# Optimization experiments

Measured on AMD Instinct MI355X. Metric: run time of the kernel, lower is better.

## Reference

```python
import jax, jax.numpy as jnp
import numpy as np

N = 100000          # total nodes
G = 128             # number of graphs
D_IN, D_H, D_OUT = 512, 1024, 512
E = 1600000         # edges (unused by the math, matches forward signature)


def setup_inputs() -> dict:
    key = jax.random.key(0)
    ks = jax.random.split(key, 9)
    x = jax.random.normal(ks[0], (N, D_IN), dtype=jnp.float32)
    edge_index = jax.random.randint(ks[1], (2, E), 0, N, dtype=jnp.int64)
    # sorted batch ids; guarantee every graph id appears at least once
    batch = jnp.sort(jnp.concatenate([
        jnp.arange(G, dtype=jnp.int64),
        jax.random.randint(ks[2], (N - G,), 0, G, dtype=jnp.int64),
    ]))
    s = 0.02
    W0 = jax.random.normal(ks[3], (D_IN, D_H), dtype=jnp.float32) * s
    b0 = jnp.zeros((D_H,), dtype=jnp.float32)
    W1 = jax.random.normal(ks[4], (D_H, D_H), dtype=jnp.float32) * s
    b1 = jnp.zeros((D_H,), dtype=jnp.float32)
    W2 = jax.random.normal(ks[5], (D_H, D_OUT), dtype=jnp.float32) * s
    b2 = jnp.zeros((D_OUT,), dtype=jnp.float32)
    return {"x": x, "edge_index": edge_index, "batch": batch,
            "W0": W0, "b0": b0, "W1": W1, "b1": b1, "W2": W2, "b2": b2}


def reference(x, edge_index, batch, W0, b0, W1, b1, W2, b2):
    # Linear + ReLU stack (dropout p=0 -> identity in eval). edge_index is unused,
    # matching the original module (its 'GCN' layer is a plain nn.Linear).
    h = jax.nn.relu(x @ W0 + b0)
    h = jax.nn.relu(h @ W1 + b1)
    h = jax.nn.relu(h @ W2 + b2)        # [N, D_OUT]
    # global mean pool per graph: fused segment-sum replaces the per-graph mask loop
    sums = jax.ops.segment_sum(h, batch, num_segments=G)                 # [G, D_OUT]
    counts = jax.ops.segment_sum(jnp.ones((h.shape[0],), h.dtype), batch,
                                 num_segments=G)                          # [G]
    return sums / counts[:, None]
```

## Files before the change

### kernel.cpp

```cpp
#include <hip/hip_runtime.h>
#include <cstdint>
#include <cstddef>

typedef __bf16 bf16x8 __attribute__((ext_vector_type(8)));
typedef float f32x4 __attribute__((ext_vector_type(4)));

__device__ __forceinline__ unsigned short f2bf(float f) {
  unsigned u = __float_as_uint(f);
  u += 0x7fffu + ((u >> 16) & 1u);
  return (unsigned short)(u >> 16);
}
__device__ __forceinline__ float bf2f(unsigned short s) {
  return __uint_as_float(((unsigned)s) << 16);
}

__device__ __forceinline__ void gld_lds16(const void* g, void* l) {
  __builtin_amdgcn_global_load_lds(
      (const __attribute__((address_space(1))) void*)g,
      (__attribute__((address_space(3))) void*)l, 16, 0, 0);
}

#define BARM() do { __builtin_amdgcn_s_barrier(); asm volatile("" ::: "memory"); } while (0)
#define VMCNT(n) asm volatile("s_waitcnt vmcnt(" #n ")" ::: "memory")
#define LGKM0()  do { asm volatile("s_waitcnt lgkmcnt(0)" ::: "memory"); \
                      __builtin_amdgcn_sched_barrier(0); } while (0)

__global__ void pack_w(const float* __restrict__ w, unsigned short* __restrict__ wp,
                       int K, int N) {
  __shared__ float tile[32][33];
  int nt32 = N >> 5;
  int bx = blockIdx.x % nt32;
  int by = blockIdx.x / nt32;
  int tx = threadIdx.x & 31, ty = threadIdx.x >> 5;
#pragma unroll
  for (int r = 0; r < 32; r += 8)
    tile[ty + r][tx] = w[(size_t)(by * 32 + ty + r) * N + bx * 32 + tx];
  __syncthreads();
  int KQ = K >> 5;
  int flat = threadIdx.x * 4;
  int c = flat >> 9;
  int l = (flat >> 3) & 63;
  int e0 = flat & 7;
  int nl = c * 16 + (l & 15);
  int kl = (l >> 4) * 8 + e0;
  unsigned short* o = wp + ((size_t)((bx * 2 + c) * KQ + by) * 64 + l) * 8 + e0;
#pragma unroll
  for (int e = 0; e < 4; ++e) o[e] = f2bf(tile[kl + e][nl]);
}

__global__ void cvt_x(const float* __restrict__ x, unsigned short* __restrict__ xb,
                      int rows, int nvalid, int D) {
  size_t total = (size_t)rows * D / 8;
  for (size_t i = (size_t)blockIdx.x * blockDim.x + threadIdx.x; i < total;
       i += (size_t)gridDim.x * blockDim.x) {
    size_t e = i * 8;
    int row = (int)(e / (size_t)D);
    uint4 ov;
    if (row < nvalid) {
      const float4* s = (const float4*)(x + e);
      float4 v0 = s[0], v1 = s[1];
      ov.x = (unsigned)f2bf(v0.x) | ((unsigned)f2bf(v0.y) << 16);
      ov.y = (unsigned)f2bf(v0.z) | ((unsigned)f2bf(v0.w) << 16);
      ov.z = (unsigned)f2bf(v1.x) | ((unsigned)f2bf(v1.y) << 16);
      ov.w = (unsigned)f2bf(v1.z) | ((unsigned)f2bf(v1.w) << 16);
    } else {
      ov.x = ov.y = ov.z = ov.w = 0u;
    }
    *(uint4*)(xb + e) = ov;
  }
}

__device__ __forceinline__ bf16x8 read_frag(const unsigned short* region, int row, int kel) {
  int ke = kel ^ (((row >> 1) & 3) << 3);
  return *(const bf16x8*)(region + row * 32 + ke);
}

__device__ __forceinline__ void stage_a(const unsigned short* gpanel, int K, int kofs,
                                        unsigned short* region, int tid) {
#pragma unroll
  for (int r = 0; r < 4; ++r) {
    int row = r * 64 + (tid >> 2);
    int ke = ((tid & 3) * 8) ^ (((row >> 1) & 3) << 3);
    gld_lds16(gpanel + (size_t)row * K + kofs + ke, region + r * 2048 + tid * 8);
  }
}

__device__ __forceinline__ void load_b4(const unsigned short* wpb, int KQ, int kq, int l,
                                        bf16x8* b) {
#pragma unroll
  for (int nn = 0; nn < 4; ++nn)
    b[nn] = *(const bf16x8*)(wpb + ((size_t)(nn * KQ + kq) * 64 + l) * 8);
}

__global__ __launch_bounds__(256, 2) void gemm_blds(
    const unsigned short* __restrict__ A,
    const unsigned short* __restrict__ Wp,
    const float* __restrict__ bias,
    unsigned short* __restrict__ C,
    int N, int K) {
  __shared__ alignas(16) unsigned short lds[2][8192];
  const int tid = threadIdx.x;
  const int w = tid >> 6, l = tid & 63;
  const int wm = w >> 1, wn = w & 1;
  const int lc = l & 15, lk8 = (l >> 4) * 8;

  const int nbn = N >> 7;
  const int nwg = gridDim.x;
  const int q = nwg >> 3, rr = nwg & 7;
  const int xcd = blockIdx.x & 7, ib = blockIdx.x >> 3;
  const int bswz = (xcd < rr ? xcd * (q + 1) : rr * (q + 1) + (xcd - rr) * q) + ib;
  const int bm = bswz / nbn, bn = bswz - bm * nbn;

  const unsigned short* Ap = A + (size_t)bm * 256 * K;
  const int KQ = K >> 5;
  const unsigned short* wpb = Wp + ((size_t)(bn * 8 + wn * 4) * KQ * 64) * 8;
  const int T = KQ;

  f32x4 acc[8][4] = {};
  bf16x8 a[8], bc[4], bn_[4];

  stage_a(Ap, K, 0, &lds[0][0], tid);
  load_b4(wpb, KQ, 0, l, bc);
  VMCNT(0);
  BARM();

#define TILE_BODY(TT, SRD, SWR, BCUR, BNXT)                                      \
  do {                                                                           \
    _Pragma("unroll") for (int mm = 0; mm < 8; ++mm)                             \
        a[mm] = read_frag(SRD, wm * 128 + mm * 16 + lc, lk8);                    \
    if ((TT) + 1 < T) {                                                          \
      stage_a(Ap, K, ((TT) + 1) * 32, SWR, tid);                                 \
      load_b4(wpb, KQ, (TT) + 1, l, BNXT);                                       \
    }                                                                            \
    BARM();                                                                      \
    LGKM0();                                                                     \
    __builtin_amdgcn_s_setprio(1);                                               \
    _Pragma("unroll") for (int mm = 0; mm < 8; ++mm)                             \
        _Pragma("unroll") for (int nn = 0; nn < 4; ++nn)                         \
            acc[mm][nn] = __builtin_amdgcn_mfma_f32_16x16x32_bf16(               \
                a[mm], BCUR[nn], acc[mm][nn], 0, 0, 0);                          \
    __builtin_amdgcn_s_setprio(0);                                               \
    VMCNT(0);                                                                    \
    BARM();                                                                      \
  } while (0)

  for (int t = 0; t < T; t += 2) {
    TILE_BODY(t, &lds[0][0], &lds[1][0], bc, bn_);
    if (t + 1 < T)
      TILE_BODY(t + 1, &lds[1][0], &lds[0][0], bn_, bc);
  }
#undef TILE_BODY

  unsigned short* eps = &lds[0][0];
  float bv[4];
#pragma unroll
  for (int nn = 0; nn < 4; ++nn) bv[nn] = bias[bn * 128 + wn * 64 + nn * 16 + lc];

#pragma unroll
  for (int r = 0; r < 2; ++r) {
    if (wm == r) {
#pragma unroll
      for (int mm = 0; mm < 8; ++mm) {
#pragma unroll
        for (int nn = 0; nn < 4; ++nn) {
          int lcol = wn * 64 + nn * 16 + lc;
#pragma unroll
          for (int j = 0; j < 4; ++j) {
            int lrow = mm * 16 + (l >> 4) * 4 + j;
            int g = lcol >> 3, e = lcol & 7;
            float v = fmaxf(acc[mm][nn][j] + bv[nn], 0.0f);
            eps[lrow * 128 + ((g ^ (lrow & 15)) << 3) + e] = f2bf(v);
          }
        }
      }
    }
    BARM();
#pragma unroll
    for (int it = 0; it < 8; ++it) {
      int flat = it * 256 + tid;
      int lrow = flat >> 4, cb = flat & 15;
      uint4 v = *(const uint4*)&eps[lrow * 128 + (((cb ^ (lrow & 15))) << 3)];
      *(uint4*)&C[(size_t)(bm * 256 + r * 128 + lrow) * N + bn * 128 + cb * 8] = v;
    }
    BARM();
  }
}

__global__ void pool_partial(const unsigned short* __restrict__ h2, const int* __restrict__ batch,
                             float* __restrict__ part, int n, int D, int S) {
  int g = blockIdx.x / S, sub = blockIdx.x - g * S;
  int lo, hi;
  { int a = 0, b = n; while (a < b) { int m = (a + b) >> 1; if (batch[m] < g) a = m + 1; else b = m; } lo = a; }
  { int a = lo, b = n; while (a < b) { int m = (a + b) >> 1; if (batch[m] < g + 1) a = m + 1; else b = m; } hi = a; }
  int t = threadIdx.x;
  float sx = 0.f, sy = 0.f;
  for (int r = lo + sub; r < hi; r += S) {
    unsigned v = *(const unsigned*)(h2 + (size_t)r * D + t * 2);
    sx += bf2f((unsigned short)(v & 0xffffu));
    sy += bf2f((unsigned short)(v >> 16));
  }
  float* o = part + (size_t)blockIdx.x * D + t * 2;
  o[0] = sx;
  o[1] = sy;
}

__global__ void pool_reduce(const float* __restrict__ part, const int* __restrict__ batch,
                            float* __restrict__ out, int n, int D, int S, int G) {
  int idx = blockIdx.x * blockDim.x + threadIdx.x;
  if (idx >= G * D) return;
  int g = idx / D, d = idx - g * D;
  int lo, hi;
  { int a = 0, b = n; while (a < b) { int m = (a + b) >> 1; if (batch[m] < g) a = m + 1; else b = m; } lo = a; }
  { int a = lo, b = n; while (a < b) { int m = (a + b) >> 1; if (batch[m] < g + 1) a = m + 1; else b = m; } hi = a; }
  float sum = 0.f;
  for (int k = 0; k < S; ++k) sum += part[(size_t)(g * S + k) * D + d];
  out[idx] = sum / (float)(hi - lo);
}

static inline size_t align256(size_t x) { return (x + 255) & ~(size_t)255; }

extern "C" void kernel_launch(void* const* d_in, const int* in_sizes, int n_in,
                              void* d_out, int out_size, void* d_ws, size_t ws_size,
                              hipStream_t stream) {
  const float* x = (const float*)d_in[0];
  const int* batch = (const int*)d_in[2];
  const float* W0 = (const float*)d_in[3];
  const float* b0 = (const float*)d_in[4];
  const float* W1 = (const float*)d_in[5];
  const float* b1 = (const float*)d_in[6];
  const float* W2 = (const float*)d_in[7];
  const float* b2 = (const float*)d_in[8];
  float* out = (float*)d_out;

  const int Nn = in_sizes[2];
  const int DIN = 512, DH = 1024, DOUT = 512;
  const int G = out_size / DOUT;
  const int S = 8;
  const int Mpad = ((Nn + 255) / 256) * 256;

  uint8_t* p = (uint8_t*)d_ws;
  unsigned short* W0p = (unsigned short*)p; p += align256((size_t)DH * DIN * 2);
  unsigned short* W1p = (unsigned short*)p; p += align256((size_t)DH * DH * 2);
  unsigned short* W2p = (unsigned short*)p; p += align256((size_t)DOUT * DH * 2);
  unsigned short* h2  = (unsigned short*)p; p += align256((size_t)Mpad * DOUT * 2);
  float* part         = (float*)p;          p += align256((size_t)G * S * DOUT * 4);
  size_t used = (size_t)(p - (uint8_t*)d_ws);
  size_t avail = ws_size > used ? ws_size - used : 0;
  size_t per_row = (size_t)(DIN + DH + DH) * 2;
  long long chl = (long long)(avail / per_row);
  chl = (chl / 256) * 256;
  int CH = (int)(chl < 256 ? 256 : chl);
  if (CH > Mpad) CH = Mpad;
  unsigned short* xb = (unsigned short*)p; p += align256((size_t)CH * DIN * 2);
  unsigned short* h0 = (unsigned short*)p; p += align256((size_t)CH * DH * 2);
  unsigned short* h1 = (unsigned short*)p; p += align256((size_t)CH * DH * 2);

  pack_w<<<dim3((DH / 32) * (DIN / 32)), 256, 0, stream>>>(W0, W0p, DIN, DH);
  pack_w<<<dim3((DH / 32) * (DH / 32)), 256, 0, stream>>>(W1, W1p, DH, DH);
  pack_w<<<dim3((DOUT / 32) * (DH / 32)), 256, 0, stream>>>(W2, W2p, DH, DOUT);

  for (int off = 0; off < Mpad; off += CH) {
    int rows = Mpad - off; if (rows > CH) rows = CH;
    int nvalid = Nn - off;
    size_t cvt_threads = (size_t)rows * DIN / 8;
    int cvt_blocks = (int)((cvt_threads + 255) / 256);
    if (cvt_blocks > 2048) cvt_blocks = 2048;
    cvt_x<<<dim3(cvt_blocks), 256, 0, stream>>>(x + (size_t)off * DIN, xb, rows, nvalid, DIN);

    gemm_blds<<<dim3((rows / 256) * (DH / 128)), 256, 0, stream>>>(xb, W0p, b0, h0, DH, DIN);
    gemm_blds<<<dim3((rows / 256) * (DH / 128)), 256, 0, stream>>>(h0, W1p, b1, h1, DH, DH);
    gemm_blds<<<dim3((rows / 256) * (DOUT / 128)), 256, 0, stream>>>(
        h1, W2p, b2, h2 + (size_t)off * DOUT, DOUT, DH);
  }

  pool_partial<<<dim3(G * S), 256, 0, stream>>>(h2, batch, part, Nn, DOUT, S);
  pool_reduce<<<dim3((G * DOUT + 255) / 256), 256, 0, stream>>>(part, batch, out, Nn, DOUT, S, G);
}
```

Before: 756.4 us.

## Widen GEMM K-tile to 64 and split B-fragment prefetch within each tile

The bf16 MFMA GEMM now stages a 256x64 A panel per iteration instead of 256x32. The LDS swizzle is adjusted to a row&7 XOR pattern, and the LDS buffers double to 64KB per block. Each iteration runs two 32-wide MFMA passes. The B-fragment register loads are interleaved between them, and fine-grained vmcnt waits replace the old full drain. This cuts barriers and full pipeline stalls per unit of K. The cost is higher LDS use per block, which could limit occupancy, and more delicate wait-count ordering.

```diff
diff --git a/kernel.cpp b/kernel.cpp
--- a/kernel.cpp
+++ b/kernel.cpp
@@ -70,18 +70,18 @@
   }
 }
 
-__device__ __forceinline__ bf16x8 read_frag(const unsigned short* region, int row, int kel) {
-  int ke = kel ^ (((row >> 1) & 3) << 3);
-  return *(const bf16x8*)(region + row * 32 + ke);
-}
-
-__device__ __forceinline__ void stage_a(const unsigned short* gpanel, int K, int kofs,
-                                        unsigned short* region, int tid) {
-#pragma unroll
-  for (int r = 0; r < 4; ++r) {
-    int row = r * 64 + (tid >> 2);
-    int ke = ((tid & 3) * 8) ^ (((row >> 1) & 3) << 3);
-    gld_lds16(gpanel + (size_t)row * K + kofs + ke, region + r * 2048 + tid * 8);
+__device__ __forceinline__ bf16x8 read_frag64(const unsigned short* region, int row, int kel) {
+  int ke = kel ^ ((row & 7) << 3);
+  return *(const bf16x8*)(region + row * 64 + ke);
+}
+
+__device__ __forceinline__ void stage_a64(const unsigned short* gpanel, int K, int kofs,
+                                          unsigned short* region, int tid) {
+#pragma unroll
+  for (int p = 0; p < 8; ++p) {
+    int row = p * 32 + (tid >> 3);
+    int ke = ((tid & 7) * 8) ^ ((row & 7) << 3);
+    gld_lds16(gpanel + (size_t)row * K + kofs + ke, region + p * 2048 + tid * 8);
   }
 }
 
@@ -92,13 +92,23 @@
     b[nn] = *(const bf16x8*)(wpb + ((size_t)(nn * KQ + kq) * 64 + l) * 8);
 }
 
-__global__ __launch_bounds__(256, 2) void gemm_blds(
+#define MFMA32(BV)                                                              \
+  do {                                                                          \
+    __builtin_amdgcn_s_setprio(1);                                              \
+    _Pragma("unroll") for (int mm = 0; mm < 8; ++mm)                            \
+        _Pragma("unroll") for (int nn = 0; nn < 4; ++nn)                        \
+            acc[mm][nn] = __builtin_amdgcn_mfma_f32_16x16x32_bf16(              \
+                a[mm], BV[nn], acc[mm][nn], 0, 0, 0);                           \
+    __builtin_amdgcn_s_setprio(0);                                              \
+  } while (0)
+
+__global__ __launch_bounds__(256, 2) void gemm_bk64(
     const unsigned short* __restrict__ A,
     const unsigned short* __restrict__ Wp,
     const float* __restrict__ bias,
     unsigned short* __restrict__ C,
     int N, int K) {
-  __shared__ alignas(16) unsigned short lds[2][8192];
+  __shared__ alignas(16) unsigned short lds[2][16384];
   const int tid = threadIdx.x;
   const int w = tid >> 6, l = tid & 63;
   const int wm = w >> 1, wn = w & 1;
@@ -114,42 +124,37 @@
   const unsigned short* Ap = A + (size_t)bm * 256 * K;
   const int KQ = K >> 5;
   const unsigned short* wpb = Wp + ((size_t)(bn * 8 + wn * 4) * KQ * 64) * 8;
-  const int T = KQ;
+  const int T = K >> 6;
 
   f32x4 acc[8][4] = {};
   bf16x8 a[8], bc[4], bn_[4];
 
-  stage_a(Ap, K, 0, &lds[0][0], tid);
+  stage_a64(Ap, K, 0, &lds[0][0], tid);
   load_b4(wpb, KQ, 0, l, bc);
   VMCNT(0);
   BARM();
 
-#define TILE_BODY(TT, SRD, SWR, BCUR, BNXT)                                      \
-  do {                                                                           \
-    _Pragma("unroll") for (int mm = 0; mm < 8; ++mm)                             \
-        a[mm] = read_frag(SRD, wm * 128 + mm * 16 + lc, lk8);                    \
-    if ((TT) + 1 < T) {                                                          \
-      stage_a(Ap, K, ((TT) + 1) * 32, SWR, tid);                                 \
-      load_b4(wpb, KQ, (TT) + 1, l, BNXT);                                       \
-    }                                                                            \
-    BARM();                                                                      \
-    LGKM0();                                                                     \
-    __builtin_amdgcn_s_setprio(1);                                               \
-    _Pragma("unroll") for (int mm = 0; mm < 8; ++mm)                             \
-        _Pragma("unroll") for (int nn = 0; nn < 4; ++nn)                         \
-            acc[mm][nn] = __builtin_amdgcn_mfma_f32_16x16x32_bf16(               \
-                a[mm], BCUR[nn], acc[mm][nn], 0, 0, 0);                          \
-    __builtin_amdgcn_s_setprio(0);                                               \
-    VMCNT(0);                                                                    \
-    BARM();                                                                      \
-  } while (0)
-
-  for (int t = 0; t < T; t += 2) {
-    TILE_BODY(t, &lds[0][0], &lds[1][0], bc, bn_);
-    if (t + 1 < T)
-      TILE_BODY(t + 1, &lds[1][0], &lds[0][0], bn_, bc);
-  }
-#undef TILE_BODY
+  for (int t = 0; t < T; ++t) {
+    const int s = t & 1;
+    const unsigned short* As = &lds[s][0];
+    unsigned short* Sn = &lds[s ^ 1][0];
+
+#pragma unroll
+    for (int mm = 0; mm < 8; ++mm) a[mm] = read_frag64(As, wm * 128 + mm * 16 + lc, lk8);
+    if (t + 1 < T) stage_a64(Ap, K, (t + 1) * 64, Sn, tid);
+    load_b4(wpb, KQ, 2 * t + 1, l, bn_);
+    if (t + 1 < T) { VMCNT(12); } else { VMCNT(4); }
+    LGKM0();
+    MFMA32(bc);
+
+#pragma unroll
+    for (int mm = 0; mm < 8; ++mm) a[mm] = read_frag64(As, wm * 128 + mm * 16 + lc, 32 + lk8);
+    if (t + 1 < T) load_b4(wpb, KQ, 2 * t + 2, l, bc);
+    if (t + 1 < T) { VMCNT(4); } else { VMCNT(0); }
+    LGKM0();
+    MFMA32(bn_);
+    BARM();
+  }
 
   unsigned short* eps = &lds[0][0];
   float bv[4];
@@ -267,9 +272,9 @@
     if (cvt_blocks > 2048) cvt_blocks = 2048;
     cvt_x<<<dim3(cvt_blocks), 256, 0, stream>>>(x + (size_t)off * DIN, xb, rows, nvalid, DIN);
 
-    gemm_blds<<<dim3((rows / 256) * (DH / 128)), 256, 0, stream>>>(xb, W0p, b0, h0, DH, DIN);
-    gemm_blds<<<dim3((rows / 256) * (DH / 128)), 256, 0, stream>>>(h0, W1p, b1, h1, DH, DH);
-    gemm_blds<<<dim3((rows / 256) * (DOUT / 128)), 256, 0, stream>>>(
+    gemm_bk64<<<dim3((rows / 256) * (DH / 128)), 256, 0, stream>>>(xb, W0p, b0, h0, DH, DIN);
+    gemm_bk64<<<dim3((rows / 256) * (DH / 128)), 256, 0, stream>>>(h0, W1p, b1, h1, DH, DH);
+    gemm_bk64<<<dim3((rows / 256) * (DOUT / 128)), 256, 0, stream>>>(
         h1, W2p, b2, h2 + (size_t)off * DOUT, DOUT, DH);
   }
 
```

Measured after the change: 732.1 us. 1.03x faster.
